# Kernel tuning notes

Measured on AMD Instinct MI355X. Metric: run time of the kernel, lower is better.

Reference implementation:

```python
import jax, jax.numpy as jnp
import numpy as np

KERNEL_SIZE = 2
TEMPERATURE = 1.0
EPS = 1e-5


def _ln(y, g, b):
    mu = jnp.mean(y, axis=-1, keepdims=True)
    var = jnp.mean((y - mu) ** 2, axis=-1, keepdims=True)
    return g * (y - mu) * jax.lax.rsqrt(var + EPS) + b


def _window_sum_before(h, k):
    # sum of h shifted right by 1..k (zero padded), matching get_hidden_states_before
    B, L, H = h.shape
    out = jnp.zeros_like(h)
    for s in range(1, k + 1):
        out = out + jnp.pad(h, ((0, 0), (s, 0), (0, 0)))[:, :L, :]
    return out


def _window_sum_after(h, k):
    B, L, H = h.shape
    out = jnp.zeros_like(h)
    for s in range(1, k + 1):
        out = out + jnp.pad(h, ((0, 0), (0, s), (0, 0)))[:, s:, :]
    return out


def setup_inputs():
    H, B, L = 512, 8, 1024
    std = 0.1
    key = jax.random.key(0)
    ks = jax.random.split(key, 12)
    return {
        "word_inputs": jax.random.normal(ks[0], (B, L, H), jnp.float32),
        "mask": jnp.zeros((B, L), jnp.float32),  # 1 = padding
        "num_layers": 3,
        "Wg": std * jax.random.normal(ks[1], (4 * H, 8 * H), jnp.float32),
        "bg": std * jax.random.normal(ks[2], (8 * H,), jnp.float32),
        "Wemb": std * jax.random.normal(ks[3], (H, 8 * H), jnp.float32),
        "Wdg": std * jax.random.normal(ks[4], (2 * H, 2 * H), jnp.float32),
        "bdg": std * jax.random.normal(ks[5], (2 * H,), jnp.float32),
        "Wdf": std * jax.random.normal(ks[6], (2 * H, H), jnp.float32),
        "bdf": std * jax.random.normal(ks[7], (H,), jnp.float32),
        "Wet": std * jax.random.normal(ks[8], (H, H), jnp.float32),
        "bet": jnp.zeros((H,), jnp.float32),
        "W1": std * jax.random.normal(ks[9], (H, 2 * H), jnp.float32),
        "b1": jnp.zeros((2 * H,), jnp.float32),
        "W2": std * jax.random.normal(ks[10], (2 * H, H), jnp.float32),
        "b2": jnp.zeros((H,), jnp.float32),
        "ln_g": jnp.ones((11, H), jnp.float32),   # order: i,o,l,f1,f2,f3,f4,gd,go,gf,h
        "ln_b": jnp.zeros((11, H), jnp.float32),
    }


def reference(word_inputs, mask, num_layers, Wg, bg, Wemb, Wdg, bdg, Wdf, bdf,
              Wet, bet, W1, b1, W2, b2, ln_g, ln_b):
    B, L, H = word_inputs.shape
    seq_mask = (1.0 - mask)[:, :, None]          # (B,L,1), 1 = real token
    softmax_neg = (-mask * 1e25)[:, :, None]     # (B,L,1)
    lens = jnp.sum(seq_mask, axis=1)             # (B,1)

    x = word_inputs * seq_mask
    h, c = x, x
    dh = jnp.sum(h, axis=1) / lens               # (B,H) dummy/sentence node
    dc = jnp.sum(c, axis=1) / lens

    we_cat = x @ Wemb                            # (B,L,8H) embedding gate terms
    emb_tr = jnp.tanh(x @ Wet + bet)             # (B,L,H)

    # dummy-gate weight chunks, mirroring torch chunk/split layout
    gWxd, gWhd = Wdg[:H, :H], Wdg[H:, :H]
    gWxo, gWho = Wdg[:H, H:], Wdg[H:, H:]
    gbd, gbo = bdg[:H], bdg[H:]
    gWxf, gWhf = Wdf[:H], Wdf[H:]

    for _ in range(num_layers):
        hb = _window_sum_before(h, KERNEL_SIZE) * seq_mask
        ha = _window_sum_after(h, KERNEL_SIZE) * seq_mask
        cb = _window_sum_before(c, KERNEL_SIZE) * seq_mask
        ca = _window_sum_after(c, KERNEL_SIZE) * seq_mask
        d_in = jnp.broadcast_to(dh[:, None, :], (B, L, H))

        # single fused 4H -> 8H gate GEMM plus precomputed embedding gates
        gates = jnp.concatenate([h, hb, ha, d_in], axis=-1) @ Wg + bg + we_cat
        fl, fr, fc_, fd, gi, ge, gw, go = jnp.split(gates, 8, axis=-1)

        g_fl = jax.nn.sigmoid(_ln(fl, ln_g[3], ln_b[3]))
        g_fr = jax.nn.sigmoid(_ln(fr, ln_g[4], ln_b[4]))
        g_fc = jax.nn.sigmoid(_ln(fc_, ln_g[5], ln_b[5]))
        g_fd = jax.nn.sigmoid(_ln(fd, ln_g[6], ln_b[6]))
        g_i = jax.nn.sigmoid(_ln(gi, ln_g[0], ln_b[0]))
        g_e = jax.nn.sigmoid(_ln(ge, ln_g[2], ln_b[2]))
        g_o = jax.nn.sigmoid(_ln(go, ln_g[1], ln_b[1]))
        cand = jnp.tanh(gw)

        # normalize the five write sources across gates (S-LSTM softmax combination)
        five = jax.nn.softmax(
            jnp.stack([g_fl, g_fr, g_fc, g_fd, g_i], axis=0) / TEMPERATURE, axis=0)
        c_new = (five[0] * cb + five[1] * ca + five[2] * c
                 + five[3] * dc[:, None, :] + five[4] * cand)
        h_new = g_o * jnp.tanh(c_new) + g_e * emb_tr

        h = h_new * seq_mask
        c = c_new * seq_mask

        # dummy (sentence-level) node update with position softmax attention
        avg_h = jnp.sum(h, axis=1) / lens
        g_d = jax.nn.sigmoid(_ln(dh @ gWxd + avg_h @ gWhd + gbd, ln_g[7], ln_b[7]))
        g_do = jax.nn.sigmoid(_ln(dh @ gWxo + avg_h @ gWho + gbo, ln_g[8], ln_b[8]))
        g_f = jax.nn.sigmoid(_ln((dh @ gWxf)[:, None, :] + h @ gWhf + bdf,
                                 ln_g[9], ln_b[9]))          # (B,L,H)
        scores = jax.nn.softmax(
            jnp.concatenate([g_f + softmax_neg, g_d[:, None, :]], axis=1)
            / TEMPERATURE, axis=1)                            # (B,L+1,H)
        dc = jnp.sum(scores[:, :L] * c, axis=1) + scores[:, L] * dc
        dh = g_do * jnp.tanh(dc)

    # position-wise FFN + residual + final LayerNorm (dropout off / eval mode)
    out = h + (jnp.maximum(h @ W1 + b1, 0.0) @ W2 + b2)
    out = _ln(out, ln_g[10], ln_b[10])
    return out * seq_mask
```

## Files before the change

kernel.cpp:

```cpp
#include <hip/hip_runtime.h>
#include <hip/hip_bf16.h>

typedef __hip_bfloat16 bf16;
typedef __attribute__((ext_vector_type(8))) short bf16x8;
typedef __attribute__((ext_vector_type(4))) float f32x4;

#define B_ 8
#define L_ 1024
#define H_ 512
#define BL_ (B_ * L_)
#define BLH_ ((size_t)BL_ * H_)
#define NCH 32
#define CHL (L_ / NCH)
#define NLAYERS 3

__device__ __forceinline__ float b2f(bf16 x) { return __bfloat162float(x); }
__device__ __forceinline__ bf16  f2b(float x) { return __float2bfloat16(x); }
__device__ __forceinline__ short f2bs(float x) { bf16 h = f2b(x); return *(short*)&h; }
__device__ __forceinline__ float bsf(short s) {
    union { unsigned int i; float f; } u; u.i = ((unsigned int)(unsigned short)s) << 16; return u.f;
}
__device__ __forceinline__ float sigm(float x) { return 1.f / (1.f + expf(-x)); }

__device__ __forceinline__ void gload16(const void* g, void* l) {
    __builtin_amdgcn_global_load_lds((const __attribute__((address_space(1))) void*)g,
                                     (__attribute__((address_space(3))) void*)l, 16, 0, 0);
}


__global__ __launch_bounds__(256) void cvtT_k(const float* __restrict__ src, bf16* __restrict__ dst,
                                              int R, int C, int ldD, int co) {
    __shared__ float t[32][33];
    int tx = threadIdx.x & 31, ty = threadIdx.x >> 5;
    int c = blockIdx.x * 32 + tx;
    int rb = blockIdx.y * 32;
    #pragma unroll
    for (int i = 0; i < 4; ++i)
        t[ty + i * 8][tx] = src[(size_t)(rb + ty + i * 8) * C + c];
    __syncthreads();
    #pragma unroll
    for (int i = 0; i < 4; ++i)
        dst[(size_t)(blockIdx.x * 32 + ty + i * 8) * ldD + co + rb + tx] = f2b(t[tx][ty + i * 8]);
}

__global__ __launch_bounds__(256) void init_k(const float* __restrict__ word, const float* __restrict__ mask,
                                              bf16* __restrict__ xbf, bf16* __restrict__ h0, bf16* __restrict__ c0,
                                              bf16* __restrict__ A) {
    size_t idx = (size_t)blockIdx.x * 256 + threadIdx.x;
    if (idx >= BLH_) return;
    int bl = (int)(idx >> 9);
    int hh = (int)(idx & 511);
    float sm = 1.f - mask[bl];
    bf16 w = f2b(word[idx] * sm);
    xbf[idx] = w; h0[idx] = w; c0[idx] = w;
    A[((size_t)bl << 11) + 1536 + hh] = w;
}

__global__ __launch_bounds__(256) void lens_k(const float* __restrict__ mask, float* __restrict__ lens) {
    __shared__ float sr[4];
    int b = blockIdx.x, t = threadIdx.x;
    float s = 0.f;
    for (int l = t; l < L_; l += 256) s += 1.f - mask[b * L_ + l];
    #pragma unroll
    for (int off = 32; off > 0; off >>= 1) s += __shfl_down(s, off);
    if ((t & 63) == 0) sr[t >> 6] = s;
    __syncthreads();
    if (t == 0) lens[b] = sr[0] + sr[1] + sr[2] + sr[3];
}

__global__ __launch_bounds__(512) void colsum_k(const bf16* __restrict__ src, float* __restrict__ partial) {
    int h = threadIdx.x, ch = blockIdx.x, b = blockIdx.y;
    float s = 0.f;
    #pragma unroll 4
    for (int i = 0; i < CHL; ++i)
        s += b2f(src[((size_t)(b * L_ + ch * CHL + i) << 9) + h]);
    partial[((size_t)(b * NCH + ch) << 9) + h] = s;
}

__global__ __launch_bounds__(512) void avgcomb_k(const float* __restrict__ partial, const float* __restrict__ lens,
                                                 float* __restrict__ o1, float* __restrict__ o2) {
    int h = threadIdx.x, b = blockIdx.x;
    float s = 0.f;
    #pragma unroll
    for (int ch = 0; ch < NCH; ++ch) s += partial[((size_t)(b * NCH + ch) << 9) + h];
    float a = s / lens[b];
    o1[(b << 9) + h] = a;
    if (o2) o2[(b << 9) + h] = a;
}

__global__ __launch_bounds__(512) void dhg_k(const float* __restrict__ dh, const bf16* __restrict__ WdhT,
                                             const float* __restrict__ bg, float* __restrict__ dhG) {
    __shared__ float a[512];
    int t = threadIdx.x, b = blockIdx.y;
    a[t] = dh[(b << 9) + t];
    __syncthreads();
    int n = blockIdx.x * 512 + t;
    const bf16* wr = WdhT + (size_t)n * 512;
    float acc = bg[n];
    #pragma unroll 8
    for (int i = 0; i < 64; ++i) {
        bf16x8 w = *(const bf16x8*)(wr + i * 8);
        #pragma unroll
        for (int j = 0; j < 8; ++j) acc = fmaf(a[i * 8 + j], bsf(w[j]), acc);
    }
    dhG[(size_t)b * 4096 + n] = acc;
}


__global__ __launch_bounds__(256) void gemm_mfma_k(const bf16* __restrict__ A, const bf16* __restrict__ Bt,
                                                   const float* __restrict__ bias, const float* __restrict__ addB,
                                                   bf16* __restrict__ C, int M, int N, int K, int mode) {
    __shared__ __align__(16) bf16 As[128 * 32];
    __shared__ __align__(16) bf16 Bs[128 * 32];
    const int tid = threadIdx.x;
    const int lane = tid & 63, wv = tid >> 6;
    const int wm = wv >> 1, wn = wv & 1;
    const int m0 = blockIdx.y * 128, n0 = blockIdx.x * 128;

    const int r0 = tid >> 2, c0 = (tid & 3) * 8;
    const bf16* Ar0 = A + (size_t)(m0 + r0) * K + c0;
    const bf16* Ar1 = A + (size_t)(m0 + r0 + 64) * K + c0;
    const bf16* Br0 = Bt + (size_t)(n0 + r0) * K + c0;
    const bf16* Br1 = Bt + (size_t)(n0 + r0 + 64) * K + c0;
    bf16* lA0 = As + (size_t)tid * 8;
    bf16* lA1 = As + (size_t)(tid + 256) * 8;
    bf16* lB0 = Bs + (size_t)tid * 8;
    bf16* lB1 = Bs + (size_t)(tid + 256) * 8;

    f32x4 acc[4][4] = {};
    const int fr = lane & 15, fq = lane >> 4;
    const bf16* aP = As + (size_t)(wm * 64 + fr) * 32 + fq * 8;
    const bf16* bP = Bs + (size_t)(wn * 64 + fr) * 32 + fq * 8;

    for (int k0 = 0; k0 < K; k0 += 32) {
        gload16(Ar0 + k0, lA0);
        gload16(Ar1 + k0, lA1);
        gload16(Br0 + k0, lB0);
        gload16(Br1 + k0, lB1);
        __syncthreads();
        bf16x8 af[4], bfr[4];
        #pragma unroll
        for (int i = 0; i < 4; ++i) {
            af[i]  = *(const bf16x8*)(aP + (size_t)i * 16 * 32);
            bfr[i] = *(const bf16x8*)(bP + (size_t)i * 16 * 32);
        }
        #pragma unroll
        for (int i = 0; i < 4; ++i)
            #pragma unroll
            for (int j = 0; j < 4; ++j)
                acc[i][j] = __builtin_amdgcn_mfma_f32_16x16x32_bf16(af[i], bfr[j], acc[i][j], 0, 0, 0);
        __syncthreads();
    }
    const float* abp = addB ? addB + (size_t)(m0 >> 10) * N : nullptr;
    #pragma unroll
    for (int j = 0; j < 4; ++j) {
        int n = n0 + wn * 64 + j * 16 + fr;
        float bb = bias ? bias[n] : 0.f;
        if (abp) bb += abp[n];
        #pragma unroll
        for (int i = 0; i < 4; ++i) {
            #pragma unroll
            for (int r = 0; r < 4; ++r) {
                int m = m0 + wm * 64 + i * 16 + fq * 4 + r;
                float v = acc[i][j][r] + bb;
                if (mode == 1) v = fmaxf(v, 0.f);
                else if (mode == 2) v = tanhf(v);
                C[(size_t)m * N + n] = f2b(v);
            }
        }
    }
}


__global__ __launch_bounds__(256) void buildA_k(const bf16* __restrict__ h,
                                                const float* __restrict__ mask, bf16* __restrict__ A) {
    int i = blockIdx.x * 256 + threadIdx.x;
    int h8 = i & 63, bl = i >> 6;
    int l = bl & 1023;
    float sm = 1.f - mask[bl];
    size_t src = ((size_t)bl << 9) + (h8 << 3);
    bf16x8 hv = *(const bf16x8*)(h + src);
    float hb[8] = {}, ha[8] = {};
    if (l >= 1) { bf16x8 v = *(const bf16x8*)(h + src - 512);
        #pragma unroll
        for (int e = 0; e < 8; ++e) hb[e] += bsf(v[e]); }
    if (l >= 2) { bf16x8 v = *(const bf16x8*)(h + src - 1024);
        #pragma unroll
        for (int e = 0; e < 8; ++e) hb[e] += bsf(v[e]); }
    if (l <= L_ - 2) { bf16x8 v = *(const bf16x8*)(h + src + 512);
        #pragma unroll
        for (int e = 0; e < 8; ++e) ha[e] += bsf(v[e]); }
    if (l <= L_ - 3) { bf16x8 v = *(const bf16x8*)(h + src + 1024);
        #pragma unroll
        for (int e = 0; e < 8; ++e) ha[e] += bsf(v[e]); }
    bf16x8 hbv, hav;
    #pragma unroll
    for (int e = 0; e < 8; ++e) { hbv[e] = f2bs(hb[e] * sm); hav[e] = f2bs(ha[e] * sm); }
    size_t base = ((size_t)bl << 11) + (h8 << 3);
    *(bf16x8*)(A + base)        = hv;
    *(bf16x8*)(A + base + 512)  = hbv;
    *(bf16x8*)(A + base + 1024) = hav;
}

__global__ __launch_bounds__(256) void fuse_k(const bf16* __restrict__ gates,
                                              const float* __restrict__ lng, const float* __restrict__ lnb,
                                              const bf16* __restrict__ cin, const bf16* __restrict__ emb,
                                              const float* __restrict__ mask, const float* __restrict__ dc,
                                              bf16* __restrict__ hout, bf16* __restrict__ cout) {
    const int lane = threadIdx.x & 63;
    const int bl = (blockIdx.x << 2) + (threadIdx.x >> 6);
    const int l = bl & 1023, b = bl >> 10;
    const float sm = 1.f - mask[bl];
    const int e0 = lane << 3;
    const bf16* gp = gates + ((size_t)bl << 12) + e0;
    float g[8][8];
    #pragma unroll
    for (int j = 0; j < 8; ++j) {
        bf16x8 v = *(const bf16x8*)(gp + (j << 9));
        #pragma unroll
        for (int i = 0; i < 8; ++i) g[j][i] = bsf(v[i]);
    }
    const int js[7]  = {0, 1, 2, 3, 4, 5, 7};
    const int lis[7] = {3, 4, 5, 6, 0, 2, 1};
    #pragma unroll
    for (int jj = 0; jj < 7; ++jj) {
        const int j = js[jj];
        float s = 0.f, q = 0.f;
        #pragma unroll
        for (int i = 0; i < 8; ++i) { s += g[j][i]; q += g[j][i] * g[j][i]; }
        #pragma unroll
        for (int off = 32; off > 0; off >>= 1) { s += __shfl_xor(s, off); q += __shfl_xor(q, off); }
        float mu = s * (1.f / 512.f);
        float rs = rsqrtf(q * (1.f / 512.f) - mu * mu + 1e-5f);
        float gmv[8], btv[8];
        const float* gm = lng + lis[jj] * 512 + e0;
        const float* bt = lnb + lis[jj] * 512 + e0;
        *(float4*)&gmv[0] = *(const float4*)gm;       *(float4*)&gmv[4] = *(const float4*)(gm + 4);
        *(float4*)&btv[0] = *(const float4*)bt;       *(float4*)&btv[4] = *(const float4*)(bt + 4);
        #pragma unroll
        for (int i = 0; i < 8; ++i)
            g[j][i] = sigm(gmv[i] * (g[j][i] - mu) * rs + btv[i]);
    }
    size_t ci = ((size_t)bl << 9) + e0;
    float cm[8] = {}, cp[8] = {}, ccv[8], ev[8], dcv[8];
    {
        bf16x8 v = *(const bf16x8*)(cin + ci);
        #pragma unroll
        for (int i = 0; i < 8; ++i) ccv[i] = bsf(v[i]);
    }
    if (l >= 1) { bf16x8 v = *(const bf16x8*)(cin + ci - 512);
        #pragma unroll
        for (int i = 0; i < 8; ++i) cm[i] += bsf(v[i]); }
    if (l >= 2) { bf16x8 v = *(const bf16x8*)(cin + ci - 1024);
        #pragma unroll
        for (int i = 0; i < 8; ++i) cm[i] += bsf(v[i]); }
    if (l <= L_ - 2) { bf16x8 v = *(const bf16x8*)(cin + ci + 512);
        #pragma unroll
        for (int i = 0; i < 8; ++i) cp[i] += bsf(v[i]); }
    if (l <= L_ - 3) { bf16x8 v = *(const bf16x8*)(cin + ci + 1024);
        #pragma unroll
        for (int i = 0; i < 8; ++i) cp[i] += bsf(v[i]); }
    {
        bf16x8 v = *(const bf16x8*)(emb + ci);
        #pragma unroll
        for (int i = 0; i < 8; ++i) ev[i] = bsf(v[i]);
    }
    *(float4*)&dcv[0] = *(const float4*)(dc + (b << 9) + e0);
    *(float4*)&dcv[4] = *(const float4*)(dc + (b << 9) + e0 + 4);
    bf16x8 hv, cv;
    #pragma unroll
    for (int i = 0; i < 8; ++i) {
        float mx = fmaxf(fmaxf(fmaxf(g[0][i], g[1][i]), fmaxf(g[2][i], g[3][i])), g[4][i]);
        float w0 = expf(g[0][i] - mx), w1 = expf(g[1][i] - mx), w2 = expf(g[2][i] - mx);
        float w3 = expf(g[3][i] - mx), w4 = expf(g[4][i] - mx);
        float inv = 1.f / (w0 + w1 + w2 + w3 + w4);
        float cand = tanhf(g[6][i]);
        float cn = (w0 * cm[i] * sm + w1 * cp[i] * sm + w2 * ccv[i] + w3 * dcv[i] + w4 * cand) * inv;
        float hn = g[7][i] * tanhf(cn) + g[5][i] * ev[i];
        hv[i] = f2bs(hn * sm);
        cv[i] = f2bs(cn * sm);
    }
    *(bf16x8*)(hout + ci) = hv;
    *(bf16x8*)(cout + ci) = cv;
}

__global__ __launch_bounds__(512) void dgu_k(const float* __restrict__ dh, const float* __restrict__ avgh,
                                             const bf16* __restrict__ WdgT, const float* __restrict__ bdg,
                                             const bf16* __restrict__ WdfT0, const float* __restrict__ bdf,
                                             const float* __restrict__ lng, const float* __restrict__ lnb,
                                             float* __restrict__ gd, float* __restrict__ gdo, float* __restrict__ u) {
    __shared__ float a2[1024];
    __shared__ float sred[16];
    int t = threadIdx.x, bx = blockIdx.x, b = blockIdx.y;
    a2[t] = dh[(b << 9) + t];
    a2[512 + t] = avgh[(b << 9) + t];
    __syncthreads();
    if (bx == 2) {
        const bf16* wr = WdfT0 + (size_t)t * 512;
        float acc = bdf[t];
        #pragma unroll 8
        for (int i = 0; i < 64; ++i) {
            bf16x8 w = *(const bf16x8*)(wr + i * 8);
            #pragma unroll
            for (int j = 0; j < 8; ++j) acc = fmaf(a2[i * 8 + j], bsf(w[j]), acc);
        }
        u[(b << 9) + t] = acc;
        return;
    }
    int col = (bx << 9) + t;
    const bf16* wr = WdgT + (size_t)col * 1024;
    float acc = bdg[col];
    #pragma unroll 8
    for (int i = 0; i < 128; ++i) {
        bf16x8 w = *(const bf16x8*)(wr + i * 8);
        #pragma unroll
        for (int j = 0; j < 8; ++j) acc = fmaf(a2[i * 8 + j], bsf(w[j]), acc);
    }
    float s = acc, q = acc * acc;
    #pragma unroll
    for (int off = 32; off > 0; off >>= 1) { s += __shfl_down(s, off); q += __shfl_down(q, off); }
    int w = t >> 6;
    if ((t & 63) == 0) { sred[w] = s; sred[8 + w] = q; }
    __syncthreads();
    float S = 0.f, Q = 0.f;
    #pragma unroll
    for (int i = 0; i < 8; ++i) { S += sred[i]; Q += sred[8 + i]; }
    float mu = S * (1.f / 512.f);
    float var = Q * (1.f / 512.f) - mu * mu;
    int li = 7 + bx;
    float n = lng[li * 512 + t] * (acc - mu) * rsqrtf(var + 1e-5f) + lnb[li * 512 + t];
    float g = sigm(n);
    if (bx) gdo[(b << 9) + t] = g; else gd[(b << 9) + t] = g;
}

__global__ __launch_bounds__(256) void gfln_k(bf16* __restrict__ gf, const float* __restrict__ lng,
                                              const float* __restrict__ lnb) {
    const int lane = threadIdx.x & 63;
    const int bl = (blockIdx.x << 2) + (threadIdx.x >> 6);
    const int e0 = lane << 3;
    size_t ci = ((size_t)bl << 9) + e0;
    float v[8];
    {
        bf16x8 gv = *(const bf16x8*)(gf + ci);
        #pragma unroll
        for (int i = 0; i < 8; ++i) v[i] = bsf(gv[i]);
    }
    float s = 0.f, q = 0.f;
    #pragma unroll
    for (int i = 0; i < 8; ++i) { s += v[i]; q += v[i] * v[i]; }
    #pragma unroll
    for (int off = 32; off > 0; off >>= 1) { s += __shfl_xor(s, off); q += __shfl_xor(q, off); }
    float mu = s * (1.f / 512.f);
    float rs = rsqrtf(q * (1.f / 512.f) - mu * mu + 1e-5f);
    float gmv[8], btv[8];
    const float* gm = lng + 9 * 512 + e0;
    const float* bt = lnb + 9 * 512 + e0;
    *(float4*)&gmv[0] = *(const float4*)gm;  *(float4*)&gmv[4] = *(const float4*)(gm + 4);
    *(float4*)&btv[0] = *(const float4*)bt;  *(float4*)&btv[4] = *(const float4*)(bt + 4);
    bf16x8 ov;
    #pragma unroll
    for (int i = 0; i < 8; ++i) ov[i] = f2bs(sigm(gmv[i] * (v[i] - mu) * rs + btv[i]));
    *(bf16x8*)(gf + ci) = ov;
}

__global__ __launch_bounds__(512) void attnp_k(const bf16* __restrict__ gf, const float* __restrict__ mask,
                                               const bf16* __restrict__ cc, float* __restrict__ pm,
                                               float* __restrict__ ps, float* __restrict__ pa) {
    int h = threadIdx.x, ch = blockIdx.x, b = blockIdx.y;
    float m = -INFINITY, s = 0.f, acc = 0.f;
    for (int i = 0; i < CHL; ++i) {
        int l = ch * CHL + i;
        size_t idx = ((size_t)(b * L_ + l) << 9) + h;
        float v = b2f(gf[idx]) - mask[b * L_ + l] * 1e25f;
        float mn = fmaxf(m, v);
        float sc = expf(m - mn);
        float p = expf(v - mn);
        s = s * sc + p;
        acc = acc * sc + p * b2f(cc[idx]);
        m = mn;
    }
    size_t o = ((size_t)(b * NCH + ch) << 9) + h;
    pm[o] = m; ps[o] = s; pa[o] = acc;
}

__global__ __launch_bounds__(512) void attnc_k(const float* __restrict__ pm, const float* __restrict__ ps,
                                               const float* __restrict__ pa, const float* __restrict__ gd,
                                               const float* __restrict__ gdo, float* __restrict__ dc,
                                               float* __restrict__ dh) {
    int h = threadIdx.x, b = blockIdx.x;
    float M = -INFINITY, S = 0.f, A = 0.f;
    #pragma unroll
    for (int ch = 0; ch < NCH; ++ch) {
        size_t o = ((size_t)(b * NCH + ch) << 9) + h;
        float m = pm[o], s = ps[o], a = pa[o];
        float Mn = fmaxf(M, m);
        float e1 = expf(M - Mn), e2 = expf(m - Mn);
        S = S * e1 + s * e2;
        A = A * e1 + a * e2;
        M = Mn;
    }
    float v = gd[(b << 9) + h];
    float Mn = fmaxf(M, v);
    float e1 = expf(M - Mn), e2 = expf(v - Mn);
    float dcold = dc[(b << 9) + h];
    S = S * e1 + e2;
    A = A * e1 + e2 * dcold;
    float dcn = A / S;
    dc[(b << 9) + h] = dcn;
    dh[(b << 9) + h] = gdo[(b << 9) + h] * tanhf(dcn);
}

__global__ __launch_bounds__(256) void final_k(const bf16* __restrict__ hfin, const bf16* __restrict__ t2,
                                               const float* __restrict__ lng, const float* __restrict__ lnb,
                                               const float* __restrict__ mask, float* __restrict__ out) {
    const int lane = threadIdx.x & 63;
    const int bl = (blockIdx.x << 2) + (threadIdx.x >> 6);
    const int e0 = lane << 3;
    size_t ci = ((size_t)bl << 9) + e0;
    float v[8];
    {
        bf16x8 a = *(const bf16x8*)(hfin + ci);
        bf16x8 bb = *(const bf16x8*)(t2 + ci);
        #pragma unroll
        for (int i = 0; i < 8; ++i) v[i] = bsf(a[i]) + bsf(bb[i]);
    }
    float s = 0.f, q = 0.f;
    #pragma unroll
    for (int i = 0; i < 8; ++i) { s += v[i]; q += v[i] * v[i]; }
    #pragma unroll
    for (int off = 32; off > 0; off >>= 1) { s += __shfl_xor(s, off); q += __shfl_xor(q, off); }
    float mu = s * (1.f / 512.f);
    float rs = rsqrtf(q * (1.f / 512.f) - mu * mu + 1e-5f);
    float gmv[8], btv[8];
    const float* gm = lng + 10 * 512 + e0;
    const float* bt = lnb + 10 * 512 + e0;
    *(float4*)&gmv[0] = *(const float4*)gm;  *(float4*)&gmv[4] = *(const float4*)(gm + 4);
    *(float4*)&btv[0] = *(const float4*)bt;  *(float4*)&btv[4] = *(const float4*)(bt + 4);
    float sm = 1.f - mask[bl];
    float o[8];
    #pragma unroll
    for (int i = 0; i < 8; ++i) o[i] = (gmv[i] * (v[i] - mu) * rs + btv[i]) * sm;
    *(float4*)(out + ci)     = *(float4*)&o[0];
    *(float4*)(out + ci + 4) = *(float4*)&o[4];
}


extern "C" void kernel_launch(void* const* d_in, const int* in_sizes, int n_in,
                              void* d_out, int out_size, void* d_ws, size_t ws_size,
                              hipStream_t stream) {
    const float* word = (const float*)d_in[0];
    const float* mask = (const float*)d_in[1];
    const float* Wg   = (const float*)d_in[3];
    const float* bg   = (const float*)d_in[4];
    const float* Wemb = (const float*)d_in[5];
    const float* Wdg  = (const float*)d_in[6];
    const float* bdg  = (const float*)d_in[7];
    const float* Wdf  = (const float*)d_in[8];
    const float* bdf  = (const float*)d_in[9];
    const float* Wet  = (const float*)d_in[10];
    const float* bet  = (const float*)d_in[11];
    const float* W1   = (const float*)d_in[12];
    const float* b1   = (const float*)d_in[13];
    const float* W2   = (const float*)d_in[14];
    const float* b2   = (const float*)d_in[15];
    const float* lng  = (const float*)d_in[16];
    const float* lnb  = (const float*)d_in[17];
    float* out = (float*)d_out;

    char* base = (char*)d_ws;
    size_t off = 0;
    auto alloc = [&](size_t bytes) -> void* {
        void* r = base + off;
        off += (bytes + 255) & ~(size_t)255;
        return r;
    };
    bf16* h0    = (bf16*)alloc(BLH_ * 2);
    bf16* h1    = (bf16*)alloc(BLH_ * 2);
    bf16* c0    = (bf16*)alloc(BLH_ * 2);
    bf16* c1    = (bf16*)alloc(BLH_ * 2);
    bf16* xbf   = (bf16*)alloc(BLH_ * 2);
    bf16* emb   = (bf16*)alloc(BLH_ * 2);
    bf16* Abuf  = (bf16*)alloc((size_t)BL_ * 2048 * 2);
    bf16* gf    = (bf16*)alloc(BLH_ * 2);
    bf16* t1    = (bf16*)alloc((size_t)BL_ * 1024 * 2);
    bf16* t2    = (bf16*)alloc(BLH_ * 2);
    bf16* WcatT = (bf16*)alloc((size_t)4096 * 2048 * 2);
    bf16* gates = (bf16*)alloc((size_t)BL_ * 4096 * 2);
    bf16* WetT  = (bf16*)alloc((size_t)512 * 512 * 2);
    bf16* WhfT  = (bf16*)alloc((size_t)512 * 512 * 2);
    bf16* W1T   = (bf16*)alloc((size_t)1024 * 512 * 2);
    bf16* W2T   = (bf16*)alloc((size_t)512 * 1024 * 2);
    bf16* WdhT  = (bf16*)alloc((size_t)4096 * 512 * 2);
    bf16* WdgT  = (bf16*)alloc((size_t)1024 * 1024 * 2);
    bf16* WdfT0 = (bf16*)alloc((size_t)512 * 512 * 2);
    float* dhG  = (float*)alloc((size_t)B_ * 4096 * 4);
    float* pm   = (float*)alloc((size_t)B_ * NCH * H_ * 4);
    float* ps   = (float*)alloc((size_t)B_ * NCH * H_ * 4);
    float* pa   = (float*)alloc((size_t)B_ * NCH * H_ * 4);
    float* lens = (float*)alloc(B_ * 4);
    float* dh   = (float*)alloc(B_ * H_ * 4);
    float* dc   = (float*)alloc(B_ * H_ * 4);
    float* avgh = (float*)alloc(B_ * H_ * 4);
    float* gd   = (float*)alloc(B_ * H_ * 4);
    float* gdo  = (float*)alloc(B_ * H_ * 4);
    float* u    = (float*)alloc(B_ * H_ * 4);
    (void)ws_size; (void)in_sizes; (void)n_in; (void)out_size;

    cvtT_k<<<dim3(128, 48), 256, 0, stream>>>(Wg,   WcatT, 1536, 4096, 2048, 0);
    cvtT_k<<<dim3(128, 16), 256, 0, stream>>>(Wemb, WcatT,  512, 4096, 2048, 1536);
    cvtT_k<<<dim3(16, 16),  256, 0, stream>>>(Wet,  WetT,   512,  512,  512, 0);
    cvtT_k<<<dim3(16, 16),  256, 0, stream>>>(Wdf + (size_t)512 * 512, WhfT, 512, 512, 512, 0);
    cvtT_k<<<dim3(32, 16),  256, 0, stream>>>(W1,   W1T,    512, 1024,  512, 0);
    cvtT_k<<<dim3(16, 32),  256, 0, stream>>>(W2,   W2T,   1024,  512, 1024, 0);
    cvtT_k<<<dim3(128, 16), 256, 0, stream>>>(Wg + (size_t)1536 * 4096, WdhT, 512, 4096, 512, 0);
    cvtT_k<<<dim3(32, 32),  256, 0, stream>>>(Wdg,  WdgT,  1024, 1024, 1024, 0);
    cvtT_k<<<dim3(16, 16),  256, 0, stream>>>(Wdf,  WdfT0,  512,  512,  512, 0);

    const int eb = (int)((BLH_ + 255) / 256);
    init_k<<<eb, 256, 0, stream>>>(word, mask, xbf, h0, c0, Abuf);
    lens_k<<<B_, 256, 0, stream>>>(mask, lens);
    colsum_k<<<dim3(NCH, B_), 512, 0, stream>>>(xbf, pm);
    avgcomb_k<<<B_, 512, 0, stream>>>(pm, lens, dh, dc);

    gemm_mfma_k<<<dim3(4, 64), 256, 0, stream>>>(xbf, WetT, bet, nullptr, emb, BL_, 512, 512, 2);

    bf16 *hcur = h0, *ccur = c0, *hnxt = h1, *cnxt = c1;
    for (int layer = 0; layer < NLAYERS; ++layer) {
        dhg_k<<<dim3(8, B_), 512, 0, stream>>>(dh, WdhT, bg, dhG);
        buildA_k<<<(int)(BLH_ / 8 / 256), 256, 0, stream>>>(hcur, mask, Abuf);
        gemm_mfma_k<<<dim3(32, 64), 256, 0, stream>>>(Abuf, WcatT, nullptr, dhG, gates, BL_, 4096, 2048, 0);
        fuse_k<<<BL_ / 4, 256, 0, stream>>>(gates, lng, lnb, ccur, emb, mask, dc, hnxt, cnxt);
        colsum_k<<<dim3(NCH, B_), 512, 0, stream>>>(hnxt, pm);
        avgcomb_k<<<B_, 512, 0, stream>>>(pm, lens, avgh, nullptr);
        dgu_k<<<dim3(3, B_), 512, 0, stream>>>(dh, avgh, WdgT, bdg, WdfT0, bdf, lng, lnb, gd, gdo, u);
        gemm_mfma_k<<<dim3(4, 64), 256, 0, stream>>>(hnxt, WhfT, nullptr, u, gf, BL_, 512, 512, 0);
        gfln_k<<<BL_ / 4, 256, 0, stream>>>(gf, lng, lnb);
        attnp_k<<<dim3(NCH, B_), 512, 0, stream>>>(gf, mask, cnxt, pm, ps, pa);
        attnc_k<<<B_, 512, 0, stream>>>(pm, ps, pa, gd, gdo, dc, dh);
        bf16* t;
        t = hcur; hcur = hnxt; hnxt = t;
        t = ccur; ccur = cnxt; cnxt = t;
    }

    gemm_mfma_k<<<dim3(8, 64), 256, 0, stream>>>(hcur, W1T, b1, nullptr, t1, BL_, 1024, 512, 1);
    gemm_mfma_k<<<dim3(4, 64), 256, 0, stream>>>(t1, W2T, b2, nullptr, t2, BL_, 512, 1024, 0);
    final_k<<<BL_ / 4, 256, 0, stream>>>(hcur, t2, lng, lnb, mask, out);
}
```

Measured before the change: 1.375 ms.

## Double K-step per GEMM iteration and fuse small per-layer kernels

The MFMA GEMM now loads two 32-wide K slices per iteration into doubled shared buffers before one barrier pair, halving the number of synchronizations per K loop. The dh·Wdh matvec is merged into the buildA kernel as extra blocks, and the avg-combine step is folded into dgu_k, removing two kernel launches per layer. The cost is more shared memory per GEMM block, which may reduce occupancy, and the avg reduction is now redundantly computed by each dgu block.

```diff
diff --git a/kernel.cpp b/kernel.cpp
--- a/kernel.cpp
+++ b/kernel.cpp
@@ -88,30 +88,12 @@
     if (o2) o2[(b << 9) + h] = a;
 }
 
-__global__ __launch_bounds__(512) void dhg_k(const float* __restrict__ dh, const bf16* __restrict__ WdhT,
-                                             const float* __restrict__ bg, float* __restrict__ dhG) {
-    __shared__ float a[512];
-    int t = threadIdx.x, b = blockIdx.y;
-    a[t] = dh[(b << 9) + t];
-    __syncthreads();
-    int n = blockIdx.x * 512 + t;
-    const bf16* wr = WdhT + (size_t)n * 512;
-    float acc = bg[n];
-    #pragma unroll 8
-    for (int i = 0; i < 64; ++i) {
-        bf16x8 w = *(const bf16x8*)(wr + i * 8);
-        #pragma unroll
-        for (int j = 0; j < 8; ++j) acc = fmaf(a[i * 8 + j], bsf(w[j]), acc);
-    }
-    dhG[(size_t)b * 4096 + n] = acc;
-}
-
 
 __global__ __launch_bounds__(256) void gemm_mfma_k(const bf16* __restrict__ A, const bf16* __restrict__ Bt,
                                                    const float* __restrict__ bias, const float* __restrict__ addB,
                                                    bf16* __restrict__ C, int M, int N, int K, int mode) {
-    __shared__ __align__(16) bf16 As[128 * 32];
-    __shared__ __align__(16) bf16 Bs[128 * 32];
+    __shared__ __align__(16) bf16 As[2 * 128 * 32];
+    __shared__ __align__(16) bf16 Bs[2 * 128 * 32];
     const int tid = threadIdx.x;
     const int lane = tid & 63, wv = tid >> 6;
     const int wm = wv >> 1, wn = wv & 1;
@@ -132,23 +114,29 @@
     const bf16* aP = As + (size_t)(wm * 64 + fr) * 32 + fq * 8;
     const bf16* bP = Bs + (size_t)(wn * 64 + fr) * 32 + fq * 8;
 
-    for (int k0 = 0; k0 < K; k0 += 32) {
-        gload16(Ar0 + k0, lA0);
-        gload16(Ar1 + k0, lA1);
-        gload16(Br0 + k0, lB0);
-        gload16(Br1 + k0, lB1);
+    for (int k0 = 0; k0 < K; k0 += 64) {
+        #pragma unroll
+        for (int h = 0; h < 2; ++h) {
+            gload16(Ar0 + k0 + h * 32, lA0 + h * 4096);
+            gload16(Ar1 + k0 + h * 32, lA1 + h * 4096);
+            gload16(Br0 + k0 + h * 32, lB0 + h * 4096);
+            gload16(Br1 + k0 + h * 32, lB1 + h * 4096);
+        }
         __syncthreads();
-        bf16x8 af[4], bfr[4];
-        #pragma unroll
-        for (int i = 0; i < 4; ++i) {
-            af[i]  = *(const bf16x8*)(aP + (size_t)i * 16 * 32);
-            bfr[i] = *(const bf16x8*)(bP + (size_t)i * 16 * 32);
+        #pragma unroll
+        for (int h = 0; h < 2; ++h) {
+            bf16x8 af[4], bfr[4];
+            #pragma unroll
+            for (int i = 0; i < 4; ++i) {
+                af[i]  = *(const bf16x8*)(aP + h * 4096 + (size_t)i * 16 * 32);
+                bfr[i] = *(const bf16x8*)(bP + h * 4096 + (size_t)i * 16 * 32);
+            }
+            #pragma unroll
+            for (int i = 0; i < 4; ++i)
+                #pragma unroll
+                for (int j = 0; j < 4; ++j)
+                    acc[i][j] = __builtin_amdgcn_mfma_f32_16x16x32_bf16(af[i], bfr[j], acc[i][j], 0, 0, 0);
         }
-        #pragma unroll
-        for (int i = 0; i < 4; ++i)
-            #pragma unroll
-            for (int j = 0; j < 4; ++j)
-                acc[i][j] = __builtin_amdgcn_mfma_f32_16x16x32_bf16(af[i], bfr[j], acc[i][j], 0, 0, 0);
         __syncthreads();
     }
     const float* abp = addB ? addB + (size_t)(m0 >> 10) * N : nullptr;
@@ -172,8 +160,31 @@
 }
 
 
-__global__ __launch_bounds__(256) void buildA_k(const bf16* __restrict__ h,
-                                                const float* __restrict__ mask, bf16* __restrict__ A) {
+#define PRE_BUILD_BLOCKS ((int)(BLH_ / 8 / 256))
+__global__ __launch_bounds__(256) void pre_k(const bf16* __restrict__ h, const float* __restrict__ mask,
+                                             bf16* __restrict__ A, const float* __restrict__ dh,
+                                             const bf16* __restrict__ WdhT, const float* __restrict__ bg,
+                                             float* __restrict__ dhG) {
+    __shared__ float a[512];
+    if (blockIdx.x >= PRE_BUILD_BLOCKS) {
+        int e = blockIdx.x - PRE_BUILD_BLOCKS;
+        int b = e >> 4, nb = e & 15;
+        int t = threadIdx.x;
+        a[t] = dh[(b << 9) + t];
+        a[t + 256] = dh[(b << 9) + t + 256];
+        __syncthreads();
+        int n = nb * 256 + t;
+        const bf16* wr = WdhT + (size_t)n * 512;
+        float acc = bg[n];
+        #pragma unroll 8
+        for (int i = 0; i < 64; ++i) {
+            bf16x8 w = *(const bf16x8*)(wr + i * 8);
+            #pragma unroll
+            for (int j = 0; j < 8; ++j) acc = fmaf(a[i * 8 + j], bsf(w[j]), acc);
+        }
+        dhG[(size_t)b * 4096 + n] = acc;
+        return;
+    }
     int i = blockIdx.x * 256 + threadIdx.x;
     int h8 = i & 63, bl = i >> 6;
     int l = bl & 1023;
@@ -284,7 +295,8 @@
     *(bf16x8*)(cout + ci) = cv;
 }
 
-__global__ __launch_bounds__(512) void dgu_k(const float* __restrict__ dh, const float* __restrict__ avgh,
+__global__ __launch_bounds__(512) void dgu_k(const float* __restrict__ dh, const float* __restrict__ partial,
+                                             const float* __restrict__ lens,
                                              const bf16* __restrict__ WdgT, const float* __restrict__ bdg,
                                              const bf16* __restrict__ WdfT0, const float* __restrict__ bdf,
                                              const float* __restrict__ lng, const float* __restrict__ lnb,
@@ -293,7 +305,12 @@
     __shared__ float sred[16];
     int t = threadIdx.x, bx = blockIdx.x, b = blockIdx.y;
     a2[t] = dh[(b << 9) + t];
-    a2[512 + t] = avgh[(b << 9) + t];
+    {
+        float s = 0.f;
+        #pragma unroll
+        for (int ch = 0; ch < NCH; ++ch) s += partial[((size_t)(b * NCH + ch) << 9) + t];
+        a2[512 + t] = s / lens[b];
+    }
     __syncthreads();
     if (bx == 2) {
         const bf16* wr = WdfT0 + (size_t)t * 512;
@@ -504,7 +521,7 @@
     float* gd   = (float*)alloc(B_ * H_ * 4);
     float* gdo  = (float*)alloc(B_ * H_ * 4);
     float* u    = (float*)alloc(B_ * H_ * 4);
-    (void)ws_size; (void)in_sizes; (void)n_in; (void)out_size;
+    (void)ws_size; (void)in_sizes; (void)n_in; (void)out_size; (void)avgh;
 
     cvtT_k<<<dim3(128, 48), 256, 0, stream>>>(Wg,   WcatT, 1536, 4096, 2048, 0);
     cvtT_k<<<dim3(128, 16), 256, 0, stream>>>(Wemb, WcatT,  512, 4096, 2048, 1536);
@@ -526,13 +543,11 @@
 
     bf16 *hcur = h0, *ccur = c0, *hnxt = h1, *cnxt = c1;
     for (int layer = 0; layer < NLAYERS; ++layer) {
-        dhg_k<<<dim3(8, B_), 512, 0, stream>>>(dh, WdhT, bg, dhG);
-        buildA_k<<<(int)(BLH_ / 8 / 256), 256, 0, stream>>>(hcur, mask, Abuf);
+        pre_k<<<PRE_BUILD_BLOCKS + 16 * B_, 256, 0, stream>>>(hcur, mask, Abuf, dh, WdhT, bg, dhG);
         gemm_mfma_k<<<dim3(32, 64), 256, 0, stream>>>(Abuf, WcatT, nullptr, dhG, gates, BL_, 4096, 2048, 0);
         fuse_k<<<BL_ / 4, 256, 0, stream>>>(gates, lng, lnb, ccur, emb, mask, dc, hnxt, cnxt);
         colsum_k<<<dim3(NCH, B_), 512, 0, stream>>>(hnxt, pm);
-        avgcomb_k<<<B_, 512, 0, stream>>>(pm, lens, avgh, nullptr);
-        dgu_k<<<dim3(3, B_), 512, 0, stream>>>(dh, avgh, WdgT, bdg, WdfT0, bdf, lng, lnb, gd, gdo, u);
+        dgu_k<<<dim3(3, B_), 512, 0, stream>>>(dh, pm, lens, WdgT, bdg, WdfT0, bdf, lng, lnb, gd, gdo, u);
         gemm_mfma_k<<<dim3(4, 64), 256, 0, stream>>>(hnxt, WhfT, nullptr, u, gf, BL_, 512, 512, 0);
         gfln_k<<<BL_ / 4, 256, 0, stream>>>(gf, lng, lnb);
         attnp_k<<<dim3(NCH, B_), 512, 0, stream>>>(gf, mask, cnxt, pm, ps, pa);
```

Measured after the change: 1.265 ms. -8.0%, faster.
